# Kernel tuning notes

Measured on AMD Instinct MI355X. Metric: run time of the kernel, lower is better.

## Reference

```python
import jax, jax.numpy as jnp
import numpy as np

N_NODES = 20000
N_EDGES = 320000
NUM_FEATURES = 128
HIDDEN = 128
NUM_CLASSES = 40
GRID_SIZE = 4
SPLINE_ORDER = 3
NB = GRID_SIZE + SPLINE_ORDER  # basis functions per input feature
_H = 2.0 / GRID_SIZE  # grid_range [-1, 1]
GRID = jnp.arange(-SPLINE_ORDER, GRID_SIZE + SPLINE_ORDER + 1, dtype=jnp.float32) * _H - 1.0


def b_splines(x):
    # x: (N, in) -> (N, in, NB) via Cox-de Boor recursion (efficient-KAN)
    xg = x[..., None]
    b = ((xg >= GRID[:-1]) & (xg < GRID[1:])).astype(x.dtype)
    for k in range(1, SPLINE_ORDER + 1):
        b = ((xg - GRID[: -(k + 1)]) / (GRID[k:-1] - GRID[: -(k + 1)]) * b[..., :-1]
             + (GRID[k + 1:] - xg) / (GRID[k + 1:] - GRID[1:-k]) * b[..., 1:])
    return b


def kan_linear(x, base_w, spline_w):
    # base branch: silu(x) @ W_base^T ; spline branch: contraction over (in, NB)
    base = jax.nn.silu(x) @ base_w.T
    spline = jnp.einsum('nik,oik->no', b_splines(x), spline_w)
    return base + spline


def gcn_conv(h, base_w, spline_w, bias, src_f, dst_f, norm):
    h = kan_linear(h, base_w, spline_w)
    msg = h[src_f] * norm[:, None]  # gather + edge scaling
    out = jax.ops.segment_sum(msg, dst_f, num_segments=N_NODES)
    return out + bias


def batchnorm(h, gamma, beta):
    mean = h.mean(axis=0)
    var = h.var(axis=0)  # biased, as torch BN uses for normalization
    return (h - mean) * jax.lax.rsqrt(var + 1e-5) * gamma + beta


def setup_inputs() -> dict:
    key = jax.random.key(0)
    ks = jax.random.split(key, 8)
    s = 0.1
    return {
        'x': jax.random.normal(ks[0], (N_NODES, NUM_FEATURES), dtype=jnp.float32),
        'edge_index': jax.random.randint(ks[1], (2, N_EDGES), 0, N_NODES, dtype=jnp.int64),
        'base_w0': jax.random.normal(ks[2], (HIDDEN, NUM_FEATURES), dtype=jnp.float32) * s,
        'spline_w0': jax.random.normal(ks[3], (HIDDEN, NUM_FEATURES, NB), dtype=jnp.float32) * s,
        'bias0': jnp.zeros((HIDDEN,), dtype=jnp.float32),
        'base_w1': jax.random.normal(ks[4], (HIDDEN, HIDDEN), dtype=jnp.float32) * s,
        'spline_w1': jax.random.normal(ks[5], (HIDDEN, HIDDEN, NB), dtype=jnp.float32) * s,
        'bias1': jnp.zeros((HIDDEN,), dtype=jnp.float32),
        'base_w_out': jax.random.normal(ks[6], (NUM_CLASSES, NUM_FEATURES + 2 * HIDDEN), dtype=jnp.float32) * s,
        'spline_w_out': jax.random.normal(ks[7], (NUM_CLASSES, NUM_FEATURES + 2 * HIDDEN, NB), dtype=jnp.float32) * s,
        'bias_out': jnp.zeros((NUM_CLASSES,), dtype=jnp.float32),
        'gamma': jnp.ones((HIDDEN,), dtype=jnp.float32),
        'beta': jnp.zeros((HIDDEN,), dtype=jnp.float32),
    }


def reference(x, edge_index, base_w0, spline_w0, bias0, base_w1, spline_w1, bias1,
              base_w_out, spline_w_out, bias_out, gamma, beta):
    # gcn_norm with self loops (computed once, reused by every layer)
    loop = jnp.arange(N_NODES, dtype=edge_index.dtype)
    src_f = jnp.concatenate([edge_index[0], loop])
    dst_f = jnp.concatenate([edge_index[1], loop])
    deg = jax.ops.segment_sum(jnp.ones_like(dst_f, dtype=x.dtype), dst_f, num_segments=N_NODES)
    dinv = jnp.where(deg > 0, jax.lax.rsqrt(jnp.maximum(deg, 1e-12)), 0.0)
    norm = dinv[src_f] * dinv[dst_f]

    skips = [x]
    h = x
    for bw, sw, b in ((base_w0, spline_w0, bias0), (base_w1, spline_w1, bias1)):
        h = gcn_conv(h, bw, sw, b, src_f, dst_f, norm)
        h = batchnorm(h, gamma, beta)  # shared BN, dropout p=0.0 is identity
        skips.append(h)
    h = jnp.concatenate(skips, axis=1)  # (N, 128 + 2*128)
    return gcn_conv(h, base_w_out, spline_w_out, bias_out, src_f, dst_f, norm)
```

## Files before the change

kernel.cpp:

```cpp
#include <hip/hip_runtime.h>

#define NN 20000

typedef _Float16 half8 __attribute__((ext_vector_type(8)));
typedef _Float16 half2v __attribute__((ext_vector_type(2)));
typedef float floatx4 __attribute__((ext_vector_type(4)));

#define MFMA16(a, b, c) __builtin_amdgcn_mfma_f32_16x16x32_f16((a), (b), (c), 0, 0, 0)
#define LD8(p) (*(const half8*)(p))
#define SBAR() __builtin_amdgcn_sched_barrier(0)

__device__ __forceinline__ void bspline7_fast(float x, float b[7]) {
  float u = (x + 2.5f) * 2.0f;
  float cf = floorf(u);
  int c = (int)cf;
  float t = u - cf;
  float omt = 1.0f - t;
  float t2 = t * t, t3 = t2 * t;
  float w0 = omt * omt * omt * (1.0f / 6.0f);
  float w1 = (3.0f * t3 - 6.0f * t2 + 4.0f) * (1.0f / 6.0f);
  float w2 = (-3.0f * t3 + 3.0f * t2 + 3.0f * t + 1.0f) * (1.0f / 6.0f);
  float w3 = t3 * (1.0f / 6.0f);
  bool valid = (c >= 0) && (c <= 9);
#pragma unroll
  for (int i = 0; i < 7; ++i) {
    int d = c - i;
    float w = (d == 0) ? w3 : (d == 1) ? w2 : (d == 2) ? w1 : (d == 3) ? w0 : 0.0f;
    b[i] = valid ? w : 0.0f;
  }
}

__device__ __forceinline__ float silu_f(float x) {
  return x * (1.0f / (1.0f + __expf(-x)));
}

__device__ __forceinline__ void build_lds16(const float* __restrict__ X,
                                            const float* __restrict__ ss, int has_bn,
                                            int row0, int tid, _Float16* __restrict__ Fs) {
#pragma unroll
  for (int it = 0; it < 8; ++it) {
    int idx = it * 256 + tid;
    int r = idx >> 7, i = idx & 127;
    float xv = X[(size_t)(row0 + r) * 128 + i];
    if (has_bn) xv = xv * ss[i] + ss[128 + i];
    float b[7];
    bspline7_fast(xv, b);
    half8 hv;
    hv[0] = (_Float16)silu_f(xv);
#pragma unroll
    for (int k = 0; k < 7; ++k) hv[k + 1] = (_Float16)b[k];
    *(half8*)(Fs + ((size_t)r * 128 + (i ^ (r & 7))) * 8) = hv;
  }
}

__global__ void packw_all(const float* __restrict__ Wb0, const float* __restrict__ Ws0,
                          const float* __restrict__ Wb1, const float* __restrict__ Ws1,
                          const float* __restrict__ WbO, const float* __restrict__ WsO,
                          _Float16* __restrict__ WPA0, _Float16* __restrict__ WPA1,
                          _Float16* __restrict__ WPC) {
  int bid = blockIdx.x;
  if (bid < 1536) {
    int s = (bid >= 768) ? 1 : 0;
    int idx = (bid - s * 768) * 256 + threadIdx.x;
    if (idx >= 196608) return;
    const float* Wb = s ? Wb1 : Wb0;
    const float* Wsp = s ? Ws1 : Ws0;
    _Float16* WP = s ? WPA1 : WPA0;
    int jj = idx & 7;
    int lane = (idx >> 3) & 63;
    int u = idx >> 9;
    int cb = u % 12, ks = u / 12;
    int i = ks * 4 + (lane >> 4);
    int orow = lane & 15;
    float v = 0.0f;
    if (cb < 8) {
      int o = cb * 16 + orow;
      v = (jj == 0) ? Wb[(size_t)o * 128 + i] : Wsp[(size_t)o * 896 + i * 7 + (jj - 1)];
    } else {
      int o = (cb - 8) * 16 + orow;
      if (o < 40)
        v = (jj == 0) ? WbO[(size_t)o * 384 + s * 128 + i]
                      : WsO[(size_t)o * 2688 + s * 896 + i * 7 + (jj - 1)];
    }
    WP[idx] = (_Float16)v;
  } else {
    int idx = (bid - 1536) * 256 + threadIdx.x;
    if (idx >= 65536) return;
    int jj = idx & 7;
    int lane = (idx >> 3) & 63;
    int u = idx >> 9;
    int cb = u & 3, ks = u >> 2;
    int i = ks * 4 + (lane >> 4);
    int o = cb * 16 + (lane & 15);
    float v = 0.0f;
    if (o < 40)
      v = (jj == 0) ? WbO[(size_t)o * 384 + 2 * 128 + i]
                    : WsO[(size_t)o * 2688 + 2 * 896 + i * 7 + (jj - 1)];
    WPC[idx] = (_Float16)v;
  }
}

__global__ void count_deg(const int* __restrict__ dst, int* __restrict__ degE, int E) {
  int e = blockIdx.x * 256 + threadIdx.x;
  if (e < E) atomicAdd(&degE[dst[e]], 1);
}

__global__ void build_meta2(const int* __restrict__ degE, int* __restrict__ rowptr,
                            int* __restrict__ cursor, float* __restrict__ dinv, int n) {
  __shared__ int wsum[16];
  int tid = threadIdx.x, lane = tid & 63, wid = tid >> 6;
  int i0 = tid * 20;
  int d[20];
  int s = 0;
#pragma unroll
  for (int j = 0; j < 20; ++j) {
    int i = i0 + j;
    int v = (i < n) ? degE[i] : 0;
    d[j] = v;
    s += v;
    if (i < n) dinv[i] = rsqrtf((float)(v + 1));
  }
  int val = s;
#pragma unroll
  for (int off = 1; off < 64; off <<= 1) {
    int t = __shfl_up(val, off);
    if (lane >= off) val += t;
  }
  if (lane == 63) wsum[wid] = val;
  __syncthreads();
  if (wid == 0) {
    int wv = (lane < 16) ? wsum[lane] : 0;
#pragma unroll
    for (int off = 1; off < 16; off <<= 1) {
      int t = __shfl_up(wv, off);
      if (lane >= off) wv += t;
    }
    if (lane < 16) wsum[lane] = wv;
  }
  __syncthreads();
  int base = (wid ? wsum[wid - 1] : 0) + val - s;
  if (tid == 0) rowptr[0] = 0;
#pragma unroll
  for (int j = 0; j < 20; ++j) {
    int i = i0 + j;
    if (i < n) {
      cursor[i] = base;
      rowptr[i + 1] = base + d[j];
      base += d[j];
    }
  }
}

__global__ void fill_csr(const int* __restrict__ src, const int* __restrict__ dst,
                         int* __restrict__ cursor, int* __restrict__ csr, int E) {
  int e = blockIdx.x * 256 + threadIdx.x;
  if (e < E) {
    int p = atomicAdd(&cursor[dst[e]], 1);
    csr[p] = src[e];
  }
}

__global__ __launch_bounds__(256) void gemmFA(const float* __restrict__ X,
                                              const float* __restrict__ ss, int has_bn,
                                              const _Float16* __restrict__ WP,
                                              const float* __restrict__ dinv,
                                              _Float16* __restrict__ A, float* __restrict__ P) {
  __shared__ _Float16 Fs[16 * 1024];
  int tid = threadIdx.x;
  int lane = tid & 63, cg = tid >> 6;
  int row0 = blockIdx.x * 16;
  build_lds16(X, ss, has_bn, row0, tid, Fs);
  __syncthreads();
  int rx = lane & 7, kg = lane >> 4;
  const _Float16* Fr = Fs + (size_t)(lane & 15) * 1024;
  const _Float16* Bp = WP + ((size_t)(cg * 3) * 64 + lane) * 8;
  floatx4 acc0 = {}, acc1 = {}, acc2 = {};
  half8 xb0 = LD8(Bp), xb1 = LD8(Bp + 512), xb2 = LD8(Bp + 1024);
  half8 yb0 = LD8(Bp + 6144), yb1 = LD8(Bp + 6144 + 512), yb2 = LD8(Bp + 6144 + 1024);
#pragma unroll 1
  for (int ks = 0; ks < 32; ks += 2) {
    half8 a0 = LD8(Fr + (size_t)((ks * 4 + kg) ^ rx) * 8);
    SBAR();
    acc0 = MFMA16(a0, xb0, acc0);
    acc1 = MFMA16(a0, xb1, acc1);
    acc2 = MFMA16(a0, xb2, acc2);
    SBAR();
    {
      const _Float16* bn = Bp + (size_t)(ks + 2) * 6144;
      xb0 = LD8(bn); xb1 = LD8(bn + 512); xb2 = LD8(bn + 1024);
    }
    half8 c0 = LD8(Fr + (size_t)(((ks + 1) * 4 + kg) ^ rx) * 8);
    SBAR();
    acc0 = MFMA16(c0, yb0, acc0);
    acc1 = MFMA16(c0, yb1, acc1);
    acc2 = MFMA16(c0, yb2, acc2);
    SBAR();
    {
      const _Float16* bn = Bp + (size_t)(ks + 3) * 6144;
      yb0 = LD8(bn); yb1 = LD8(bn + 512); yb2 = LD8(bn + 1024);
    }
    SBAR();
  }
  int oc = lane & 15;
  int r0 = row0 + (lane >> 4) * 4;
  floatx4 accs[3] = {acc0, acc1, acc2};
#pragma unroll
  for (int q = 0; q < 3; ++q) {
    int cb = cg * 3 + q;
    if (cb < 8) {
#pragma unroll
      for (int t = 0; t < 4; ++t)
        A[(size_t)(r0 + t) * 128 + cb * 16 + oc] = (_Float16)(accs[q][t] * dinv[r0 + t]);
    } else {
#pragma unroll
      for (int t = 0; t < 4; ++t) P[(size_t)(r0 + t) * 64 + (cb - 8) * 16 + oc] = accs[q][t];
    }
  }
}

__global__ __launch_bounds__(256) void gemmFC(const float* __restrict__ X,
                                              const float* __restrict__ ss,
                                              const _Float16* __restrict__ WP,
                                              const float* __restrict__ P0,
                                              const float* __restrict__ P1,
                                              const float* __restrict__ dinv,
                                              _Float16* __restrict__ C) {
  __shared__ _Float16 Fs[16 * 1024];
  int tid = threadIdx.x;
  int lane = tid & 63, cg = tid >> 6;
  int row0 = blockIdx.x * 16;
  build_lds16(X, ss, 1, row0, tid, Fs);
  __syncthreads();
  int rx = lane & 7, kg = lane >> 4;
  const _Float16* Fr = Fs + (size_t)(lane & 15) * 1024;
  const _Float16* Bp = WP + ((size_t)cg * 64 + lane) * 8;
  floatx4 acc0 = {};
  half8 xb = LD8(Bp), yb = LD8(Bp + 2048);
#pragma unroll 1
  for (int ks = 0; ks < 32; ks += 2) {
    half8 a0 = LD8(Fr + (size_t)((ks * 4 + kg) ^ rx) * 8);
    SBAR();
    acc0 = MFMA16(a0, xb, acc0);
    SBAR();
    xb = LD8(Bp + (size_t)(ks + 2) * 2048);
    half8 c0 = LD8(Fr + (size_t)(((ks + 1) * 4 + kg) ^ rx) * 8);
    SBAR();
    acc0 = MFMA16(c0, yb, acc0);
    SBAR();
    yb = LD8(Bp + (size_t)(ks + 3) * 2048);
    SBAR();
  }
  int oc = lane & 15;
  int r0 = row0 + (lane >> 4) * 4;
#pragma unroll
  for (int t = 0; t < 4; ++t) {
    size_t idx = (size_t)(r0 + t) * 64 + cg * 16 + oc;
    C[idx] = (_Float16)((acc0[t] + P0[idx] + P1[idx]) * dinv[r0 + t]);
  }
}

__global__ __launch_bounds__(256) void aggregate128h(const _Float16* __restrict__ Ah,
                                                     const int* __restrict__ rowptr,
                                                     const int* __restrict__ csr,
                                                     const float* __restrict__ dinv,
                                                     const float* __restrict__ bias,
                                                     float* __restrict__ Y) {
  int wid = threadIdx.x >> 6, lane = threadIdx.x & 63;
  int n = blockIdx.x * 4 + wid;
  float di = dinv[n];
  half2v self = *(const half2v*)(Ah + (size_t)n * 128 + lane * 2);
  float a0 = (float)self[0], a1 = (float)self[1];
  float b0x = 0, b0y = 0, b1x = 0, b1y = 0, b2x = 0, b2y = 0, b3x = 0, b3y = 0;
  int e0 = rowptr[n], m = rowptr[n + 1] - e0;
  int j = 0;
  for (; j + 4 <= m; j += 4) {
    int s0 = csr[e0 + j], s1 = csr[e0 + j + 1], s2 = csr[e0 + j + 2], s3 = csr[e0 + j + 3];
    half2v r0 = *(const half2v*)(Ah + (size_t)s0 * 128 + lane * 2);
    half2v r1 = *(const half2v*)(Ah + (size_t)s1 * 128 + lane * 2);
    half2v r2 = *(const half2v*)(Ah + (size_t)s2 * 128 + lane * 2);
    half2v r3 = *(const half2v*)(Ah + (size_t)s3 * 128 + lane * 2);
    b0x += (float)r0[0]; b0y += (float)r0[1];
    b1x += (float)r1[0]; b1y += (float)r1[1];
    b2x += (float)r2[0]; b2y += (float)r2[1];
    b3x += (float)r3[0]; b3y += (float)r3[1];
  }
  for (; j < m; ++j) {
    int s = csr[e0 + j];
    half2v r = *(const half2v*)(Ah + (size_t)s * 128 + lane * 2);
    b0x += (float)r[0]; b0y += (float)r[1];
  }
  a0 += (b0x + b1x) + (b2x + b3x);
  a1 += (b0y + b1y) + (b2y + b3y);
  float2 outv = {a0 * di + bias[lane * 2], a1 * di + bias[lane * 2 + 1]};
  *(float2*)(Y + (size_t)n * 128 + lane * 2) = outv;
}

__global__ __launch_bounds__(256) void aggregate40h(const _Float16* __restrict__ Ch,
                                                    const int* __restrict__ rowptr,
                                                    const int* __restrict__ csr,
                                                    const float* __restrict__ dinv,
                                                    const float* __restrict__ bias,
                                                    float* __restrict__ out) {
  int wid = threadIdx.x >> 6, lane = threadIdx.x & 63;
  int n = blockIdx.x * 4 + wid;
  float di = dinv[n];
  float a = (float)Ch[(size_t)n * 64 + lane];
  float b0 = 0, b1 = 0, b2 = 0, b3 = 0;
  int e0 = rowptr[n], m = rowptr[n + 1] - e0;
  int j = 0;
  for (; j + 4 <= m; j += 4) {
    int s0 = csr[e0 + j], s1 = csr[e0 + j + 1], s2 = csr[e0 + j + 2], s3 = csr[e0 + j + 3];
    b0 += (float)Ch[(size_t)s0 * 64 + lane];
    b1 += (float)Ch[(size_t)s1 * 64 + lane];
    b2 += (float)Ch[(size_t)s2 * 64 + lane];
    b3 += (float)Ch[(size_t)s3 * 64 + lane];
  }
  for (; j < m; ++j) {
    int s = csr[e0 + j];
    b0 += (float)Ch[(size_t)s * 64 + lane];
  }
  a += (b0 + b1) + (b2 + b3);
  if (lane < 40) out[(size_t)n * 40 + lane] = a * di + bias[lane];
}

__global__ __launch_bounds__(256) void bn_stats(const float* __restrict__ H,
                                                float* __restrict__ partial) {
  int tid = threadIdx.x;
  int c4 = (tid & 31) * 4;
  int r0 = blockIdx.x * 32 + (tid >> 5) * 4;
  float s0 = 0, s1 = 0, s2 = 0, s3 = 0, q0 = 0, q1 = 0, q2 = 0, q3 = 0;
#pragma unroll
  for (int j = 0; j < 4; ++j) {
    float4 v = *(const float4*)(H + (size_t)(r0 + j) * 128 + c4);
    s0 += v.x; s1 += v.y; s2 += v.z; s3 += v.w;
    q0 += v.x * v.x; q1 += v.y * v.y; q2 += v.z * v.z; q3 += v.w * v.w;
  }
  __shared__ float sh[2][256][4];
  sh[0][tid][0] = s0; sh[0][tid][1] = s1; sh[0][tid][2] = s2; sh[0][tid][3] = s3;
  sh[1][tid][0] = q0; sh[1][tid][1] = q1; sh[1][tid][2] = q2; sh[1][tid][3] = q3;
  __syncthreads();
  if (tid < 32) {
    float a0 = 0, a1 = 0, a2 = 0, a3 = 0, b0 = 0, b1 = 0, b2 = 0, b3 = 0;
#pragma unroll
    for (int g = 0; g < 8; ++g) {
      int u = g * 32 + tid;
      a0 += sh[0][u][0]; a1 += sh[0][u][1]; a2 += sh[0][u][2]; a3 += sh[0][u][3];
      b0 += sh[1][u][0]; b1 += sh[1][u][1]; b2 += sh[1][u][2]; b3 += sh[1][u][3];
    }
    float* p = partial + (size_t)blockIdx.x * 256;
    p[tid * 4 + 0] = a0; p[tid * 4 + 1] = a1; p[tid * 4 + 2] = a2; p[tid * 4 + 3] = a3;
    p[128 + tid * 4 + 0] = b0; p[128 + tid * 4 + 1] = b1;
    p[128 + tid * 4 + 2] = b2; p[128 + tid * 4 + 3] = b3;
  }
}

__global__ __launch_bounds__(256) void bn_reduce(const float* __restrict__ partial,
                                                 float* __restrict__ p2) {
  int tid = threadIdx.x;
  const float* base = partial + (size_t)blockIdx.x * 25 * 256 + tid;
  float a0 = 0, a1 = 0, a2 = 0, a3 = 0, a4 = 0;
#pragma unroll
  for (int j = 0; j < 5; ++j) {
    a0 += base[(j * 5 + 0) * 256];
    a1 += base[(j * 5 + 1) * 256];
    a2 += base[(j * 5 + 2) * 256];
    a3 += base[(j * 5 + 3) * 256];
    a4 += base[(j * 5 + 4) * 256];
  }
  p2[(size_t)blockIdx.x * 256 + tid] = ((a0 + a1) + (a2 + a3)) + a4;
}

__global__ __launch_bounds__(256) void bn_final2(const float* __restrict__ p2,
                                                 const float* __restrict__ gamma,
                                                 const float* __restrict__ beta,
                                                 float* __restrict__ ss) {
  int tid = threadIdx.x;
  double a0 = 0, a1 = 0, a2 = 0, a3 = 0, a4 = 0;
#pragma unroll
  for (int j = 0; j < 5; ++j) {
    a0 += (double)p2[(size_t)(j * 5 + 0) * 256 + tid];
    a1 += (double)p2[(size_t)(j * 5 + 1) * 256 + tid];
    a2 += (double)p2[(size_t)(j * 5 + 2) * 256 + tid];
    a3 += (double)p2[(size_t)(j * 5 + 3) * 256 + tid];
    a4 += (double)p2[(size_t)(j * 5 + 4) * 256 + tid];
  }
  double tot = ((a0 + a1) + (a2 + a3)) + a4;
  __shared__ double sh[256];
  sh[tid] = tot;
  __syncthreads();
  if (tid < 128) {
    double S = sh[tid];
    double Q = sh[128 + tid];
    double mean = S / (double)NN;
    double var = Q / (double)NN - mean * mean;
    float sc = gamma[tid] * rsqrtf((float)var + 1e-5f);
    ss[tid] = sc;
    ss[128 + tid] = beta[tid] - (float)mean * sc;
  }
}

extern "C" void kernel_launch(void* const* d_in, const int* in_sizes, int n_in,
                              void* d_out, int out_size, void* d_ws, size_t ws_size,
                              hipStream_t stream) {
  const float* x = (const float*)d_in[0];
  const int* ei = (const int*)d_in[1];
  const float* bw0 = (const float*)d_in[2];
  const float* sw0 = (const float*)d_in[3];
  const float* b0 = (const float*)d_in[4];
  const float* bw1 = (const float*)d_in[5];
  const float* sw1 = (const float*)d_in[6];
  const float* b1 = (const float*)d_in[7];
  const float* bwo = (const float*)d_in[8];
  const float* swo = (const float*)d_in[9];
  const float* bo = (const float*)d_in[10];
  const float* gamma = (const float*)d_in[11];
  const float* beta = (const float*)d_in[12];
  const int E = in_sizes[1] / 2;
  const int* esrc = ei;
  const int* edst = ei + E;

  char* ws = (char*)d_ws;
  size_t off = 0;
  auto alloc = [&](size_t bytes) -> void* {
    void* p = ws + off;
    off = (off + bytes + 255) & ~(size_t)255;
    return p;
  };
  _Float16* WPA0 = (_Float16*)alloc((196608 + 16384) * 2);
  _Float16* WPA1 = (_Float16*)alloc((196608 + 16384) * 2);
  _Float16* WPC = (_Float16*)alloc((65536 + 16384) * 2);
  float* dinv = (float*)alloc(NN * 4);
  int* degE = (int*)alloc(NN * 4);
  int* rowptr = (int*)alloc((NN + 1) * 4);
  int* cursor = (int*)alloc(NN * 4);
  int* csr = (int*)alloc((size_t)E * 4);
  _Float16* A = (_Float16*)alloc((size_t)NN * 128 * 2);
  float* h1 = (float*)alloc((size_t)NN * 128 * 4);
  float* P0 = (float*)alloc((size_t)NN * 64 * 4);
  float* P1 = (float*)alloc((size_t)NN * 64 * 4);
  _Float16* Ch = (_Float16*)alloc((size_t)NN * 64 * 2);
  float* partial = (float*)alloc((size_t)625 * 256 * 4);
  float* p2 = (float*)alloc((size_t)25 * 256 * 4);
  float* ssb = (float*)alloc(256 * 4);
  float* h2 = h1;
  (void)ws_size; (void)n_in; (void)out_size;

  int egrid = (E + 255) / 256;
  const int GG = 1250;

  hipMemsetAsync(degE, 0, NN * sizeof(int), stream);
  packw_all<<<1792, 256, 0, stream>>>(bw0, sw0, bw1, sw1, bwo, swo, WPA0, WPA1, WPC);
  count_deg<<<egrid, 256, 0, stream>>>(edst, degE, E);
  build_meta2<<<1, 1024, 0, stream>>>(degE, rowptr, cursor, dinv, NN);
  fill_csr<<<egrid, 256, 0, stream>>>(esrc, edst, cursor, csr, E);

  gemmFA<<<GG, 256, 0, stream>>>(x, ssb, 0, WPA0, dinv, A, P0);
  aggregate128h<<<5000, 256, 0, stream>>>(A, rowptr, csr, dinv, b0, h1);
  bn_stats<<<625, 256, 0, stream>>>(h1, partial);
  bn_reduce<<<25, 256, 0, stream>>>(partial, p2);
  bn_final2<<<1, 256, 0, stream>>>(p2, gamma, beta, ssb);

  gemmFA<<<GG, 256, 0, stream>>>(h1, ssb, 1, WPA1, dinv, A, P1);
  aggregate128h<<<5000, 256, 0, stream>>>(A, rowptr, csr, dinv, b1, h2);
  bn_stats<<<625, 256, 0, stream>>>(h2, partial);
  bn_reduce<<<25, 256, 0, stream>>>(partial, p2);
  bn_final2<<<1, 256, 0, stream>>>(p2, gamma, beta, ssb);

  gemmFC<<<GG, 256, 0, stream>>>(h2, ssb, WPC, P0, P1, dinv, Ch);
  aggregate40h<<<5000, 256, 0, stream>>>(Ch, rowptr, csr, dinv, bo, (float*)d_out);
}
```

Before: 248.0 us.

## Stage weight tiles in LDS via async global_load_lds, share across two row groups

```diff
diff --git a/kernel.cpp b/kernel.cpp
--- a/kernel.cpp
+++ b/kernel.cpp
@@ -8,7 +8,11 @@
 
 #define MFMA16(a, b, c) __builtin_amdgcn_mfma_f32_16x16x32_f16((a), (b), (c), 0, 0, 0)
 #define LD8(p) (*(const half8*)(p))
-#define SBAR() __builtin_amdgcn_sched_barrier(0)
+
+__device__ __forceinline__ void gl_lds16(const _Float16* g, _Float16* l) {
+  __builtin_amdgcn_global_load_lds((const __attribute__((address_space(1))) char*)g,
+                                   (__attribute__((address_space(3))) char*)l, 16, 0, 0);
+}
 
 __device__ __forceinline__ void bspline7_fast(float x, float b[7]) {
   float u = (x + 2.5f) * 2.0f;
@@ -32,25 +36,6 @@
 
 __device__ __forceinline__ float silu_f(float x) {
   return x * (1.0f / (1.0f + __expf(-x)));
-}
-
-__device__ __forceinline__ void build_lds16(const float* __restrict__ X,
-                                            const float* __restrict__ ss, int has_bn,
-                                            int row0, int tid, _Float16* __restrict__ Fs) {
-#pragma unroll
-  for (int it = 0; it < 8; ++it) {
-    int idx = it * 256 + tid;
-    int r = idx >> 7, i = idx & 127;
-    float xv = X[(size_t)(row0 + r) * 128 + i];
-    if (has_bn) xv = xv * ss[i] + ss[128 + i];
-    float b[7];
-    bspline7_fast(xv, b);
-    half8 hv;
-    hv[0] = (_Float16)silu_f(xv);
-#pragma unroll
-    for (int k = 0; k < 7; ++k) hv[k + 1] = (_Float16)b[k];
-    *(half8*)(Fs + ((size_t)r * 128 + (i ^ (r & 7))) * 8) = hv;
-  }
 }
 
 __global__ void packw_all(const float* __restrict__ Wb0, const float* __restrict__ Ws0,
@@ -160,49 +145,75 @@
   }
 }
 
-__global__ __launch_bounds__(256) void gemmFA(const float* __restrict__ X,
+__global__ __launch_bounds__(512) void gemmFA(const float* __restrict__ X,
                                               const float* __restrict__ ss, int has_bn,
                                               const _Float16* __restrict__ WP,
                                               const float* __restrict__ dinv,
                                               _Float16* __restrict__ A, float* __restrict__ P) {
-  __shared__ _Float16 Fs[16 * 1024];
+  __shared__ _Float16 Fs[32 * 1024];
+  __shared__ _Float16 Bb[3 * 12 * 512];
   int tid = threadIdx.x;
-  int lane = tid & 63, cg = tid >> 6;
-  int row0 = blockIdx.x * 16;
-  build_lds16(X, ss, has_bn, row0, tid, Fs);
+  int lane = tid & 63, wid = tid >> 6;
+  int cg = wid & 3, rg = wid >> 2;
+  int row0 = blockIdx.x * 32;
+  if (rg == 0) {
+#pragma unroll
+    for (int k = 0; k < 2; ++k)
+#pragma unroll
+      for (int q = 0; q < 3; ++q) {
+        int cb = cg * 3 + q;
+        gl_lds16(WP + (size_t)k * 6144 + cb * 512 + lane * 8, Bb + k * 6144 + cb * 512);
+      }
+  }
+#pragma unroll
+  for (int it = 0; it < 8; ++it) {
+    int idx = it * 512 + tid;
+    int r = idx >> 7, i = idx & 127;
+    float xv = X[(size_t)(row0 + r) * 128 + i];
+    if (has_bn) xv = xv * ss[i] + ss[128 + i];
+    float b[7];
+    bspline7_fast(xv, b);
+    half8 hv;
+    hv[0] = (_Float16)silu_f(xv);
+#pragma unroll
+    for (int k = 0; k < 7; ++k) hv[k + 1] = (_Float16)b[k];
+    *(half8*)(Fs + ((size_t)r * 128 + (i ^ (r & 7))) * 8) = hv;
+  }
   __syncthreads();
+
   int rx = lane & 7, kg = lane >> 4;
-  const _Float16* Fr = Fs + (size_t)(lane & 15) * 1024;
-  const _Float16* Bp = WP + ((size_t)(cg * 3) * 64 + lane) * 8;
+  const _Float16* Fr = Fs + (size_t)(rg * 16 + (lane & 15)) * 1024;
   floatx4 acc0 = {}, acc1 = {}, acc2 = {};
-  half8 xb0 = LD8(Bp), xb1 = LD8(Bp + 512), xb2 = LD8(Bp + 1024);
-  half8 yb0 = LD8(Bp + 6144), yb1 = LD8(Bp + 6144 + 512), yb2 = LD8(Bp + 6144 + 1024);
+  int rb = 0;
 #pragma unroll 1
-  for (int ks = 0; ks < 32; ks += 2) {
-    half8 a0 = LD8(Fr + (size_t)((ks * 4 + kg) ^ rx) * 8);
-    SBAR();
-    acc0 = MFMA16(a0, xb0, acc0);
-    acc1 = MFMA16(a0, xb1, acc1);
-    acc2 = MFMA16(a0, xb2, acc2);
-    SBAR();
-    {
-      const _Float16* bn = Bp + (size_t)(ks + 2) * 6144;
-      xb0 = LD8(bn); xb1 = LD8(bn + 512); xb2 = LD8(bn + 1024);
-    }
-    half8 c0 = LD8(Fr + (size_t)(((ks + 1) * 4 + kg) ^ rx) * 8);
-    SBAR();
-    acc0 = MFMA16(c0, yb0, acc0);
-    acc1 = MFMA16(c0, yb1, acc1);
-    acc2 = MFMA16(c0, yb2, acc2);
-    SBAR();
-    {
-      const _Float16* bn = Bp + (size_t)(ks + 3) * 6144;
-      yb0 = LD8(bn); yb1 = LD8(bn + 512); yb2 = LD8(bn + 1024);
-    }
-    SBAR();
-  }
+  for (int ks = 0; ks < 32; ++ks) {
+    if (rg == 0 && ks < 30) {
+      int wb = rb + 2;
+      if (wb >= 3) wb -= 3;
+      const _Float16* src = WP + (size_t)(ks + 2) * 6144 + (cg * 3) * 512 + lane * 8;
+      _Float16* dst = Bb + wb * 6144 + (cg * 3) * 512;
+      gl_lds16(src, dst);
+      gl_lds16(src + 512, dst + 512);
+      gl_lds16(src + 1024, dst + 1024);
+    }
+    const _Float16* Bc = Bb + rb * 6144 + (cg * 3) * 512 + lane * 8;
+    half8 a = LD8(Fr + (size_t)((ks * 4 + kg) ^ rx) * 8);
+    half8 b0 = LD8(Bc);
+    half8 b1 = LD8(Bc + 512);
+    half8 b2 = LD8(Bc + 1024);
+    acc0 = MFMA16(a, b0, acc0);
+    acc1 = MFMA16(a, b1, acc1);
+    acc2 = MFMA16(a, b2, acc2);
+    if (ks < 30) {
+      asm volatile("s_waitcnt vmcnt(3)\n\ts_barrier" ::: "memory");
+    } else if (ks == 30) {
+      asm volatile("s_waitcnt vmcnt(0)\n\ts_barrier" ::: "memory");
+    }
+    rb = (rb == 2) ? 0 : rb + 1;
+  }
+
   int oc = lane & 15;
-  int r0 = row0 + (lane >> 4) * 4;
+  int r0 = row0 + rg * 16 + (lane >> 4) * 4;
   floatx4 accs[3] = {acc0, acc1, acc2};
 #pragma unroll
   for (int q = 0; q < 3; ++q) {
@@ -218,40 +229,64 @@
   }
 }
 
-__global__ __launch_bounds__(256) void gemmFC(const float* __restrict__ X,
+__global__ __launch_bounds__(512) void gemmFC(const float* __restrict__ X,
                                               const float* __restrict__ ss,
                                               const _Float16* __restrict__ WP,
                                               const float* __restrict__ P0,
                                               const float* __restrict__ P1,
                                               const float* __restrict__ dinv,
                                               _Float16* __restrict__ C) {
-  __shared__ _Float16 Fs[16 * 1024];
+  __shared__ _Float16 Fs[32 * 1024];
+  __shared__ _Float16 Bb[3 * 4 * 512];
   int tid = threadIdx.x;
-  int lane = tid & 63, cg = tid >> 6;
-  int row0 = blockIdx.x * 16;
-  build_lds16(X, ss, 1, row0, tid, Fs);
+  int lane = tid & 63, wid = tid >> 6;
+  int cg = wid & 3, rg = wid >> 2;
+  int row0 = blockIdx.x * 32;
+  if (rg == 0) {
+#pragma unroll
+    for (int k = 0; k < 2; ++k)
+      gl_lds16(WP + (size_t)k * 2048 + cg * 512 + lane * 8, Bb + k * 2048 + cg * 512);
+  }
+#pragma unroll
+  for (int it = 0; it < 8; ++it) {
+    int idx = it * 512 + tid;
+    int r = idx >> 7, i = idx & 127;
+    float xv = X[(size_t)(row0 + r) * 128 + i];
+    xv = xv * ss[i] + ss[128 + i];
+    float b[7];
+    bspline7_fast(xv, b);
+    half8 hv;
+    hv[0] = (_Float16)silu_f(xv);
+#pragma unroll
+    for (int k = 0; k < 7; ++k) hv[k + 1] = (_Float16)b[k];
+    *(half8*)(Fs + ((size_t)r * 128 + (i ^ (r & 7))) * 8) = hv;
+  }
   __syncthreads();
+
   int rx = lane & 7, kg = lane >> 4;
-  const _Float16* Fr = Fs + (size_t)(lane & 15) * 1024;
-  const _Float16* Bp = WP + ((size_t)cg * 64 + lane) * 8;
+  const _Float16* Fr = Fs + (size_t)(rg * 16 + (lane & 15)) * 1024;
   floatx4 acc0 = {};
-  half8 xb = LD8(Bp), yb = LD8(Bp + 2048);
+  int rb = 0;
 #pragma unroll 1
-  for (int ks = 0; ks < 32; ks += 2) {
-    half8 a0 = LD8(Fr + (size_t)((ks * 4 + kg) ^ rx) * 8);
-    SBAR();
-    acc0 = MFMA16(a0, xb, acc0);
-    SBAR();
-    xb = LD8(Bp + (size_t)(ks + 2) * 2048);
-    half8 c0 = LD8(Fr + (size_t)(((ks + 1) * 4 + kg) ^ rx) * 8);
-    SBAR();
-    acc0 = MFMA16(c0, yb, acc0);
-    SBAR();
-    yb = LD8(Bp + (size_t)(ks + 3) * 2048);
-    SBAR();
-  }
+  for (int ks = 0; ks < 32; ++ks) {
+    if (rg == 0 && ks < 30) {
+      int wb = rb + 2;
+      if (wb >= 3) wb -= 3;
+      gl_lds16(WP + (size_t)(ks + 2) * 2048 + cg * 512 + lane * 8, Bb + wb * 2048 + cg * 512);
+    }
+    half8 a = LD8(Fr + (size_t)((ks * 4 + kg) ^ rx) * 8);
+    half8 b = LD8(Bb + rb * 2048 + cg * 512 + lane * 8);
+    acc0 = MFMA16(a, b, acc0);
+    if (ks < 30) {
+      asm volatile("s_waitcnt vmcnt(1)\n\ts_barrier" ::: "memory");
+    } else if (ks == 30) {
+      asm volatile("s_waitcnt vmcnt(0)\n\ts_barrier" ::: "memory");
+    }
+    rb = (rb == 2) ? 0 : rb + 1;
+  }
+
   int oc = lane & 15;
-  int r0 = row0 + (lane >> 4) * 4;
+  int r0 = row0 + rg * 16 + (lane >> 4) * 4;
 #pragma unroll
   for (int t = 0; t < 4; ++t) {
     size_t idx = (size_t)(r0 + t) * 64 + cg * 16 + oc;
@@ -426,9 +461,9 @@
     off = (off + bytes + 255) & ~(size_t)255;
     return p;
   };
-  _Float16* WPA0 = (_Float16*)alloc((196608 + 16384) * 2);
-  _Float16* WPA1 = (_Float16*)alloc((196608 + 16384) * 2);
-  _Float16* WPC = (_Float16*)alloc((65536 + 16384) * 2);
+  _Float16* WPA0 = (_Float16*)alloc(196608 * 2);
+  _Float16* WPA1 = (_Float16*)alloc(196608 * 2);
+  _Float16* WPC = (_Float16*)alloc(65536 * 2);
   float* dinv = (float*)alloc(NN * 4);
   int* degE = (int*)alloc(NN * 4);
   int* rowptr = (int*)alloc((NN + 1) * 4);
@@ -446,7 +481,7 @@
   (void)ws_size; (void)n_in; (void)out_size;
 
   int egrid = (E + 255) / 256;
-  const int GG = 1250;
+  const int GG = 625;
 
   hipMemsetAsync(degE, 0, NN * sizeof(int), stream);
   packw_all<<<1792, 256, 0, stream>>>(bw0, sw0, bw1, sw1, bwo, swo, WPA0, WPA1, WPC);
@@ -454,18 +489,18 @@
   build_meta2<<<1, 1024, 0, stream>>>(degE, rowptr, cursor, dinv, NN);
   fill_csr<<<egrid, 256, 0, stream>>>(esrc, edst, cursor, csr, E);
 
-  gemmFA<<<GG, 256, 0, stream>>>(x, ssb, 0, WPA0, dinv, A, P0);
+  gemmFA<<<GG, 512, 0, stream>>>(x, ssb, 0, WPA0, dinv, A, P0);
   aggregate128h<<<5000, 256, 0, stream>>>(A, rowptr, csr, dinv, b0, h1);
   bn_stats<<<625, 256, 0, stream>>>(h1, partial);
   bn_reduce<<<25, 256, 0, stream>>>(partial, p2);
   bn_final2<<<1, 256, 0, stream>>>(p2, gamma, beta, ssb);
 
-  gemmFA<<<GG, 256, 0, stream>>>(h1, ssb, 1, WPA1, dinv, A, P1);
+  gemmFA<<<GG, 512, 0, stream>>>(h1, ssb, 1, WPA1, dinv, A, P1);
   aggregate128h<<<5000, 256, 0, stream>>>(A, rowptr, csr, dinv, b1, h2);
   bn_stats<<<625, 256, 0, stream>>>(h2, partial);
   bn_reduce<<<25, 256, 0, stream>>>(partial, p2);
   bn_final2<<<1, 256, 0, stream>>>(p2, gamma, beta, ssb);
 
-  gemmFC<<<GG, 256, 0, stream>>>(h2, ssb, WPC, P0, P1, dinv, Ch);
+  gemmFC<<<GG, 512, 0, stream>>>(h2, ssb, WPC, P0, P1, dinv, Ch);
   aggregate40h<<<5000, 256, 0, stream>>>(Ch, rowptr, csr, dinv, bo, (float*)d_out);
 }
```

After: 326.3 us. 1.32x slower.

## Build spline A-fragments in registers instead of LDS in GEMM kernels

Applied to the files above, without the earlier changes.

```diff
diff --git a/kernel.cpp b/kernel.cpp
--- a/kernel.cpp
+++ b/kernel.cpp
@@ -8,7 +8,6 @@
 
 #define MFMA16(a, b, c) __builtin_amdgcn_mfma_f32_16x16x32_f16((a), (b), (c), 0, 0, 0)
 #define LD8(p) (*(const half8*)(p))
-#define SBAR() __builtin_amdgcn_sched_barrier(0)
 
 __device__ __forceinline__ void bspline7_fast(float x, float b[7]) {
   float u = (x + 2.5f) * 2.0f;
@@ -34,23 +33,14 @@
   return x * (1.0f / (1.0f + __expf(-x)));
 }
 
-__device__ __forceinline__ void build_lds16(const float* __restrict__ X,
-                                            const float* __restrict__ ss, int has_bn,
-                                            int row0, int tid, _Float16* __restrict__ Fs) {
-#pragma unroll
-  for (int it = 0; it < 8; ++it) {
-    int idx = it * 256 + tid;
-    int r = idx >> 7, i = idx & 127;
-    float xv = X[(size_t)(row0 + r) * 128 + i];
-    if (has_bn) xv = xv * ss[i] + ss[128 + i];
-    float b[7];
-    bspline7_fast(xv, b);
-    half8 hv;
-    hv[0] = (_Float16)silu_f(xv);
-#pragma unroll
-    for (int k = 0; k < 7; ++k) hv[k + 1] = (_Float16)b[k];
-    *(half8*)(Fs + ((size_t)r * 128 + (i ^ (r & 7))) * 8) = hv;
-  }
+__device__ __forceinline__ half8 afrag(float xv) {
+  float b[7];
+  bspline7_fast(xv, b);
+  half8 hv;
+  hv[0] = (_Float16)silu_f(xv);
+#pragma unroll
+  for (int k = 0; k < 7; ++k) hv[k + 1] = (_Float16)b[k];
+  return hv;
 }
 
 __global__ void packw_all(const float* __restrict__ Wb0, const float* __restrict__ Ws0,
@@ -106,9 +96,11 @@
 }
 
 __global__ void build_meta2(const int* __restrict__ degE, int* __restrict__ rowptr,
-                            int* __restrict__ cursor, float* __restrict__ dinv, int n) {
+                            int* __restrict__ cursor, float* __restrict__ dinv,
+                            float* __restrict__ ssb, int n) {
   __shared__ int wsum[16];
   int tid = threadIdx.x, lane = tid & 63, wid = tid >> 6;
+  if (tid < 256) ssb[tid] = (tid < 128) ? 1.0f : 0.0f;
   int i0 = tid * 20;
   int d[20];
   int s = 0;
@@ -160,46 +152,33 @@
   }
 }
 
-__global__ __launch_bounds__(256) void gemmFA(const float* __restrict__ X,
-                                              const float* __restrict__ ss, int has_bn,
+__global__ __launch_bounds__(512) void gemmRA(const float* __restrict__ X,
+                                              const float* __restrict__ ss,
                                               const _Float16* __restrict__ WP,
                                               const float* __restrict__ dinv,
                                               _Float16* __restrict__ A, float* __restrict__ P) {
-  __shared__ _Float16 Fs[16 * 1024];
   int tid = threadIdx.x;
-  int lane = tid & 63, cg = tid >> 6;
-  int row0 = blockIdx.x * 16;
-  build_lds16(X, ss, has_bn, row0, tid, Fs);
-  __syncthreads();
-  int rx = lane & 7, kg = lane >> 4;
-  const _Float16* Fr = Fs + (size_t)(lane & 15) * 1024;
+  int lane = tid & 63, wid = tid >> 6;
+  int rg = wid & 1, cg = wid >> 1;
+  int row0 = blockIdx.x * 32 + rg * 16;
+  int r = row0 + (lane & 15);
+  int ig = lane >> 4;
+  const float* Xp = X + (size_t)r * 128 + ig;
+  const float* S0 = ss + ig;
+  const float* S1 = ss + 128 + ig;
   const _Float16* Bp = WP + ((size_t)(cg * 3) * 64 + lane) * 8;
   floatx4 acc0 = {}, acc1 = {}, acc2 = {};
-  half8 xb0 = LD8(Bp), xb1 = LD8(Bp + 512), xb2 = LD8(Bp + 1024);
-  half8 yb0 = LD8(Bp + 6144), yb1 = LD8(Bp + 6144 + 512), yb2 = LD8(Bp + 6144 + 1024);
-#pragma unroll 1
-  for (int ks = 0; ks < 32; ks += 2) {
-    half8 a0 = LD8(Fr + (size_t)((ks * 4 + kg) ^ rx) * 8);
-    SBAR();
-    acc0 = MFMA16(a0, xb0, acc0);
-    acc1 = MFMA16(a0, xb1, acc1);
-    acc2 = MFMA16(a0, xb2, acc2);
-    SBAR();
-    {
-      const _Float16* bn = Bp + (size_t)(ks + 2) * 6144;
-      xb0 = LD8(bn); xb1 = LD8(bn + 512); xb2 = LD8(bn + 1024);
-    }
-    half8 c0 = LD8(Fr + (size_t)(((ks + 1) * 4 + kg) ^ rx) * 8);
-    SBAR();
-    acc0 = MFMA16(c0, yb0, acc0);
-    acc1 = MFMA16(c0, yb1, acc1);
-    acc2 = MFMA16(c0, yb2, acc2);
-    SBAR();
-    {
-      const _Float16* bn = Bp + (size_t)(ks + 3) * 6144;
-      yb0 = LD8(bn); yb1 = LD8(bn + 512); yb2 = LD8(bn + 1024);
-    }
-    SBAR();
+#pragma unroll 2
+  for (int ks = 0; ks < 32; ++ks) {
+    float xv = Xp[ks * 4] * S0[ks * 4] + S1[ks * 4];
+    half8 a = afrag(xv);
+    const _Float16* bq = Bp + (size_t)ks * 6144;
+    half8 b0 = LD8(bq);
+    half8 b1 = LD8(bq + 512);
+    half8 b2 = LD8(bq + 1024);
+    acc0 = MFMA16(a, b0, acc0);
+    acc1 = MFMA16(a, b1, acc1);
+    acc2 = MFMA16(a, b2, acc2);
   }
   int oc = lane & 15;
   int r0 = row0 + (lane >> 4) * 4;
@@ -218,37 +197,30 @@
   }
 }
 
-__global__ __launch_bounds__(256) void gemmFC(const float* __restrict__ X,
+__global__ __launch_bounds__(512) void gemmRC(const float* __restrict__ X,
                                               const float* __restrict__ ss,
                                               const _Float16* __restrict__ WP,
                                               const float* __restrict__ P0,
                                               const float* __restrict__ P1,
                                               const float* __restrict__ dinv,
                                               _Float16* __restrict__ C) {
-  __shared__ _Float16 Fs[16 * 1024];
   int tid = threadIdx.x;
-  int lane = tid & 63, cg = tid >> 6;
-  int row0 = blockIdx.x * 16;
-  build_lds16(X, ss, 1, row0, tid, Fs);
-  __syncthreads();
-  int rx = lane & 7, kg = lane >> 4;
-  const _Float16* Fr = Fs + (size_t)(lane & 15) * 1024;
+  int lane = tid & 63, wid = tid >> 6;
+  int rg = wid & 1, cg = wid >> 1;
+  int row0 = blockIdx.x * 32 + rg * 16;
+  int r = row0 + (lane & 15);
+  int ig = lane >> 4;
+  const float* Xp = X + (size_t)r * 128 + ig;
+  const float* S0 = ss + ig;
+  const float* S1 = ss + 128 + ig;
   const _Float16* Bp = WP + ((size_t)cg * 64 + lane) * 8;
   floatx4 acc0 = {};
-  half8 xb = LD8(Bp), yb = LD8(Bp + 2048);
-#pragma unroll 1
-  for (int ks = 0; ks < 32; ks += 2) {
-    half8 a0 = LD8(Fr + (size_t)((ks * 4 + kg) ^ rx) * 8);
-    SBAR();
-    acc0 = MFMA16(a0, xb, acc0);
-    SBAR();
-    xb = LD8(Bp + (size_t)(ks + 2) * 2048);
-    half8 c0 = LD8(Fr + (size_t)(((ks + 1) * 4 + kg) ^ rx) * 8);
-    SBAR();
-    acc0 = MFMA16(c0, yb, acc0);
-    SBAR();
-    yb = LD8(Bp + (size_t)(ks + 3) * 2048);
-    SBAR();
+#pragma unroll 2
+  for (int ks = 0; ks < 32; ++ks) {
+    float xv = Xp[ks * 4] * S0[ks * 4] + S1[ks * 4];
+    half8 a = afrag(xv);
+    half8 b = LD8(Bp + (size_t)ks * 2048);
+    acc0 = MFMA16(a, b, acc0);
   }
   int oc = lane & 15;
   int r0 = row0 + (lane >> 4) * 4;
@@ -286,8 +258,8 @@
   }
   for (; j < m; ++j) {
     int s = csr[e0 + j];
-    half2v r = *(const half2v*)(Ah + (size_t)s * 128 + lane * 2);
-    b0x += (float)r[0]; b0y += (float)r[1];
+    half2v rr = *(const half2v*)(Ah + (size_t)s * 128 + lane * 2);
+    b0x += (float)rr[0]; b0y += (float)rr[1];
   }
   a0 += (b0x + b1x) + (b2x + b3x);
   a1 += (b0y + b1y) + (b2y + b3y);
@@ -426,9 +398,9 @@
     off = (off + bytes + 255) & ~(size_t)255;
     return p;
   };
-  _Float16* WPA0 = (_Float16*)alloc((196608 + 16384) * 2);
-  _Float16* WPA1 = (_Float16*)alloc((196608 + 16384) * 2);
-  _Float16* WPC = (_Float16*)alloc((65536 + 16384) * 2);
+  _Float16* WPA0 = (_Float16*)alloc(196608 * 2);
+  _Float16* WPA1 = (_Float16*)alloc(196608 * 2);
+  _Float16* WPC = (_Float16*)alloc(65536 * 2);
   float* dinv = (float*)alloc(NN * 4);
   int* degE = (int*)alloc(NN * 4);
   int* rowptr = (int*)alloc((NN + 1) * 4);
@@ -446,26 +418,26 @@
   (void)ws_size; (void)n_in; (void)out_size;
 
   int egrid = (E + 255) / 256;
-  const int GG = 1250;
+  const int GG = 625;
 
   hipMemsetAsync(degE, 0, NN * sizeof(int), stream);
   packw_all<<<1792, 256, 0, stream>>>(bw0, sw0, bw1, sw1, bwo, swo, WPA0, WPA1, WPC);
   count_deg<<<egrid, 256, 0, stream>>>(edst, degE, E);
-  build_meta2<<<1, 1024, 0, stream>>>(degE, rowptr, cursor, dinv, NN);
+  build_meta2<<<1, 1024, 0, stream>>>(degE, rowptr, cursor, dinv, ssb, NN);
   fill_csr<<<egrid, 256, 0, stream>>>(esrc, edst, cursor, csr, E);
 
-  gemmFA<<<GG, 256, 0, stream>>>(x, ssb, 0, WPA0, dinv, A, P0);
+  gemmRA<<<GG, 512, 0, stream>>>(x, ssb, WPA0, dinv, A, P0);
   aggregate128h<<<5000, 256, 0, stream>>>(A, rowptr, csr, dinv, b0, h1);
   bn_stats<<<625, 256, 0, stream>>>(h1, partial);
   bn_reduce<<<25, 256, 0, stream>>>(partial, p2);
   bn_final2<<<1, 256, 0, stream>>>(p2, gamma, beta, ssb);
 
-  gemmFA<<<GG, 256, 0, stream>>>(h1, ssb, 1, WPA1, dinv, A, P1);
+  gemmRA<<<GG, 512, 0, stream>>>(h1, ssb, WPA1, dinv, A, P1);
   aggregate128h<<<5000, 256, 0, stream>>>(A, rowptr, csr, dinv, b1, h2);
   bn_stats<<<625, 256, 0, stream>>>(h2, partial);
   bn_reduce<<<25, 256, 0, stream>>>(partial, p2);
   bn_final2<<<1, 256, 0, stream>>>(p2, gamma, beta, ssb);
 
-  gemmFC<<<GG, 256, 0, stream>>>(h2, ssb, WPC, P0, P1, dinv, Ch);
+  gemmRC<<<GG, 512, 0, stream>>>(h2, ssb, WPC, P0, P1, dinv, Ch);
   aggregate40h<<<5000, 256, 0, stream>>>(Ch, rowptr, csr, dinv, bo, (float*)d_out);
 }
```

Result: slower. 362.7 us (+46.2%).
